# Kernel tuning notes

Measured on AMD Instinct MI355X. Metric: run time of the kernel, lower is better.

The kernel has to match this reference:

```python
import jax, jax.numpy as jnp
import numpy as np

N = 50000   # nodes
E = 800000  # edges
D = 128     # input feature dim
H = 128     # hidden dim
L = 3       # num GIN layers
G = 64      # graphs in batch


def setup_inputs() -> dict:
    key = jax.random.key(0)
    ks = jax.random.split(key, 20)
    inp = {
        "h": jax.random.normal(ks[0], (N, D), jnp.float32),
        "src": jax.random.randint(ks[1], (E,), 0, N),
        "dst": jax.random.randint(ks[2], (E,), 0, N),
        "graph_ids": jnp.sort(jax.random.randint(ks[3], (N,), 0, G)),
    }
    k = 4
    for i in range(L):
        in_dim = D if i == 0 else H
        inp[f"w1_{i}"] = jax.random.normal(ks[k], (in_dim, H), jnp.float32) / np.sqrt(in_dim).astype(np.float32); k += 1
        inp[f"b1_{i}"] = jnp.zeros((H,), jnp.float32)
        inp[f"w2_{i}"] = jax.random.normal(ks[k], (H, H), jnp.float32) / np.sqrt(H).astype(np.float32); k += 1
        inp[f"b2_{i}"] = jnp.zeros((H,), jnp.float32)
    inp["w_out"] = jax.random.normal(ks[k], (H * L, 1), jnp.float32) / np.sqrt(H * L).astype(np.float32)
    inp["b_out"] = jnp.zeros((1,), jnp.float32)
    return inp


def _gin_layer(h, src, dst, w1, b1, w2, b2):
    # sum aggregation over edges: agg[i] = sum_{(j->i) in E} h[j]
    agg = jax.ops.segment_sum(h[src], dst, num_segments=N)
    z = h + agg  # (1 + eps) * h + agg with eps = 0 (DGL GINConv default)
    return jax.nn.relu(z @ w1 + b1) @ w2 + b2  # 2-layer MLP


def reference(h, src, dst, graph_ids,
              w1_0, b1_0, w2_0, b2_0,
              w1_1, b1_1, w2_1, b2_1,
              w1_2, b1_2, w2_2, b2_2,
              w_out, b_out):
    layers = [(w1_0, b1_0, w2_0, b2_0),
              (w1_1, b1_1, w2_1, b2_1),
              (w1_2, b1_2, w2_2, b2_2)]
    readouts = []
    for w1, b1, w2, b2 in layers:
        h = _gin_layer(h, src, dst, w1, b1, w2, b2)
        # per-graph sum readout of node features: [G, H]
        readouts.append(jax.ops.segment_sum(h, graph_ids, num_segments=G))
    hg = jnp.concatenate(readouts, axis=1)  # [G, H*L]
    return hg @ w_out + b_out  # [G, 1]
```

## Files before the change

### kernel.cpp

```cpp
#include <hip/hip_runtime.h>

#define NN 50000
#define NE 800000
#define DIMH 128
#define NGRAPH 64
#define NTILES 3125
#define PAIRS 1024
#define MLP_BLOCKS 512
#define MLP_ITERS 4
#define NBIN 196
#define BCAP 8064

typedef __attribute__((ext_vector_type(8))) short bf16x8;
typedef __attribute__((ext_vector_type(4))) float f32x4;

__device__ __forceinline__ unsigned short f2b(float f) {
  unsigned int b = __float_as_uint(f);
  unsigned int r = (b + 0x7FFFu + ((b >> 16) & 1u)) >> 16;
  return (unsigned short)r;
}
__device__ __forceinline__ float b2f_lo(unsigned int u) { return __uint_as_float(u << 16); }
__device__ __forceinline__ float b2f_hi(unsigned int u) { return __uint_as_float(u & 0xffff0000u); }


__global__ void zero_int_kernel(int* __restrict__ p, int n) {
  int i = blockIdx.x * 256 + threadIdx.x;
  if (i < n) p[i] = 0;
}

__global__ __launch_bounds__(256) void bin_scatter_kernel(const int* __restrict__ src,
                                                          const int* __restrict__ dst,
                                                          int* __restrict__ gcnt,
                                                          int2* __restrict__ staging) {
  __shared__ int hist[NBIN];
  __shared__ int base[NBIN];
  int tid = threadIdx.x;
  for (int i = tid; i < NBIN; i += 256) hist[i] = 0;
  __syncthreads();
  int e0 = blockIdx.x * 2048;
  int2 ed[8];
  int bin[8], rank[8];
#pragma unroll
  for (int k = 0; k < 8; ++k) {
    int e = e0 + k * 256 + tid;
    bin[k] = 0; rank[k] = 0; ed[k] = make_int2(0, 0);
    if (e < NE) {
      ed[k].x = src[e]; ed[k].y = dst[e];
      bin[k] = ed[k].y >> 8;
      rank[k] = atomicAdd(&hist[bin[k]], 1);
    }
  }
  __syncthreads();
  for (int i = tid; i < NBIN; i += 256) base[i] = atomicAdd(&gcnt[i], hist[i]);
  __syncthreads();
#pragma unroll
  for (int k = 0; k < 8; ++k) {
    int e = e0 + k * 256 + tid;
    if (e < NE) staging[bin[k] * BCAP + base[bin[k]] + rank[k]] = ed[k];
  }
}

__global__ __launch_bounds__(256) void bin_fill_kernel(const int2* __restrict__ staging,
                                                       const int* __restrict__ gcnt,
                                                       int* __restrict__ bucket,
                                                       int* __restrict__ cnt) {
  __shared__ int h[256];
  int b = blockIdx.x;
  int tid = threadIdx.x;
  h[tid] = 0;
  __syncthreads();
  int n = gcnt[b];
  for (int i = tid; i < n; i += 256) {
    int2 e = staging[b * BCAP + i];
    int local = e.y & 255;
    int r = atomicAdd(&h[local], 1);
    if (r < 64) bucket[(b * 256 + local) * 64 + r] = e.x;
  }
  __syncthreads();
  int node = b * 256 + tid;
  if (node < NN) cnt[node] = h[tid];
}


__global__ void convw_kernel(const float* __restrict__ w, unsigned short* __restrict__ wt) {
  int i = blockIdx.x * 256 + threadIdx.x;
  int c = i >> 7, k = i & 127;
  wt[i] = f2b(w[k * DIMH + c]);
}

__global__ void convh_kernel(const float* __restrict__ h, unsigned int* __restrict__ o) {
  int i = blockIdx.x * 256 + threadIdx.x;
  float2 v = ((const float2*)h)[i];
  o[i] = (unsigned int)f2b(v.x) | ((unsigned int)f2b(v.y) << 16);
}


__global__ void agg_kernel(const uint2* __restrict__ hp, const int* __restrict__ cnt,
                           const int* __restrict__ bucket, uint2* __restrict__ z) {
  int gidx = blockIdx.x * 256 + threadIdx.x;
  int node = gidx >> 6;
  int lane = gidx & 63;
  int half = lane >> 5;
  int l5 = lane & 31;
  int c = cnt[node];
  if (c > 64) c = 64;
  int idx = bucket[node * 64 + lane];

  uint2 own = hp[node * 32 + l5];
  float a0 = b2f_lo(own.x), a1 = b2f_hi(own.x), a2 = b2f_lo(own.y), a3 = b2f_hi(own.y);
  if (half) { a0 = 0.f; a1 = 0.f; a2 = 0.f; a3 = 0.f; }

  int j = 0;
  for (; j + 8 <= c; j += 8) {
#pragma unroll
    for (int k = 0; k < 4; ++k) {
      int nb = __shfl(idx, j + 2 * k + half, 64);
      uint2 u = hp[nb * 32 + l5];
      a0 += b2f_lo(u.x); a1 += b2f_hi(u.x);
      a2 += b2f_lo(u.y); a3 += b2f_hi(u.y);
    }
  }
  for (; j < c; j += 2) {
    int slot = j + half;
    int s2 = slot < c ? slot : 0;
    int nb = __shfl(idx, s2, 64);
    uint2 u = hp[nb * 32 + l5];
    float m = slot < c ? 1.f : 0.f;
    a0 += m * b2f_lo(u.x); a1 += m * b2f_hi(u.x);
    a2 += m * b2f_lo(u.y); a3 += m * b2f_hi(u.y);
  }

  a0 += __shfl_xor(a0, 32, 64);
  a1 += __shfl_xor(a1, 32, 64);
  a2 += __shfl_xor(a2, 32, 64);
  a3 += __shfl_xor(a3, 32, 64);

  if (half == 0) {
    uint2 o;
    o.x = (unsigned int)f2b(a0) | ((unsigned int)f2b(a1) << 16);
    o.y = (unsigned int)f2b(a2) | ((unsigned int)f2b(a3) << 16);
    z[node * 32 + l5] = o;
  }
}

__global__ __launch_bounds__(256, 2) void mlp_kernel(const unsigned short* __restrict__ X,
                                                     const unsigned short* __restrict__ W1t,
                                                     const float* __restrict__ b1,
                                                     const unsigned short* __restrict__ W2t,
                                                     const float* __restrict__ b2,
                                                     unsigned short* __restrict__ Y,
                                                     const int* __restrict__ gids,
                                                     const float* __restrict__ wout,
                                                     float* __restrict__ gout) {
  __shared__ unsigned short y1[2][2][2048];
  __shared__ float s_gout[NGRAPH];
  int tid = threadIdx.x;
  if (tid < NGRAPH) s_gout[tid] = 0.f;

  int wv = tid >> 6;
  int lane = tid & 63;
  int pb = wv >> 1;
  int half = wv & 1;
  int l15 = lane & 15;
  int g = lane >> 4;
  int p = blockIdx.x * 2 + pb;

  bf16x8 a[4];
  {
    const unsigned short* xb = X + (p * 16 + l15) * DIMH + g * 8;
#pragma unroll
    for (int kt = 0; kt < 4; ++kt) a[kt] = *(const bf16x8*)(xb + kt * 32);
  }

  bf16x8 fb1[4][4], fb2[4][4];
  const unsigned short* w1b = W1t + (half * 64 + l15) * DIMH + g * 8;
  const unsigned short* w2b = W2t + (half * 64 + l15) * DIMH + g * 8;
#pragma unroll
  for (int n = 0; n < 4; ++n)
#pragma unroll
    for (int kt = 0; kt < 4; ++kt) {
      fb1[n][kt] = *(const bf16x8*)(w1b + n * 16 * DIMH + kt * 32);
      fb2[n][kt] = *(const bf16x8*)(w2b + n * 16 * DIMH + kt * 32);
    }
  float b1v[4], b2v[4], wov[4];
#pragma unroll
  for (int n = 0; n < 4; ++n) {
    int col = half * 64 + n * 16 + l15;
    b1v[n] = b1[col];
    b2v[n] = b2[col];
    wov[n] = wout[col];
  }
  __syncthreads();

#pragma unroll
  for (int i = 0; i < MLP_ITERS; ++i) {
    int rtc = p + i * PAIRS;
    bool active = rtc < NTILES;
    unsigned short* buf = y1[pb][i & 1];

    if (active) {
#pragma unroll
      for (int n = 0; n < 4; ++n) {
        f32x4 acc = (f32x4){0.f, 0.f, 0.f, 0.f};
#pragma unroll
        for (int kt = 0; kt < 4; ++kt)
          acc = __builtin_amdgcn_mfma_f32_16x16x32_bf16(a[kt], fb1[n][kt], acc, 0, 0, 0);
        int col2 = (half * 64 + n * 16 + l15) * 2;
#pragma unroll
        for (int r = 0; r < 4; ++r) {
          float f = fmaxf(acc[r] + b1v[n], 0.f);
          int row = 4 * g + r;
          buf[((row * 256 + col2) ^ (row << 4)) >> 1] = f2b(f);
        }
      }
    }

    int rtn = p + (i + 1) * PAIRS;
    if (i + 1 < MLP_ITERS && rtn < NTILES) {
      const unsigned short* xb = X + (rtn * 16 + l15) * DIMH + g * 8;
#pragma unroll
      for (int kt = 0; kt < 4; ++kt) a[kt] = *(const bf16x8*)(xb + kt * 32);
    }

    __syncthreads();

    if (active) {
      bf16x8 a2[4];
#pragma unroll
      for (int kt = 0; kt < 4; ++kt)
        a2[kt] = *(const bf16x8*)&buf[((l15 * 256 + kt * 64 + g * 16) ^ (l15 << 4)) >> 1];

      float pr[4] = {0.f, 0.f, 0.f, 0.f};
#pragma unroll
      for (int n = 0; n < 4; ++n) {
        f32x4 acc = (f32x4){0.f, 0.f, 0.f, 0.f};
#pragma unroll
        for (int kt = 0; kt < 4; ++kt)
          acc = __builtin_amdgcn_mfma_f32_16x16x32_bf16(a2[kt], fb2[n][kt], acc, 0, 0, 0);
        int col = half * 64 + n * 16 + l15;
#pragma unroll
        for (int r = 0; r < 4; ++r) {
          float f = acc[r] + b2v[n];
          if (Y) Y[(rtc * 16 + 4 * g + r) * DIMH + col] = f2b(f);
          pr[r] += f * wov[n];
        }
      }
#pragma unroll
      for (int r = 0; r < 4; ++r) {
#pragma unroll
        for (int off = 1; off < 16; off <<= 1) pr[r] += __shfl_xor(pr[r], off, 64);
      }
      if (l15 == 0) {
#pragma unroll
        for (int r = 0; r < 4; ++r)
          atomicAdd(&s_gout[gids[rtc * 16 + 4 * g + r]], pr[r]);
      }
    }
  }

  __syncthreads();
  if (tid < NGRAPH) {
    float v = s_gout[tid];
    if (v != 0.f) atomicAdd(&gout[tid], v);
  }
}

__global__ void init_out_kernel(float* __restrict__ out, const float* __restrict__ b_out) {
  int i = threadIdx.x;
  if (i < NGRAPH) out[i] = b_out[0];
}


extern "C" void kernel_launch(void* const* d_in, const int* in_sizes, int n_in,
                              void* d_out, int out_size, void* d_ws, size_t ws_size,
                              hipStream_t stream) {
  const float* h = (const float*)d_in[0];
  const int* src = (const int*)d_in[1];
  const int* dst = (const int*)d_in[2];
  const int* gids = (const int*)d_in[3];
  const float* w_out = (const float*)d_in[16];
  const float* b_out = (const float*)d_in[17];
  float* out = (float*)d_out;

  char* base = (char*)d_ws;
  unsigned int* bufH = (unsigned int*)(base);
  int2* staging = (int2*)(base + 12800000);
  unsigned int* bufC = (unsigned int*)(base + 25600000);
  int* bucket = (int*)(base + 38400000);
  int* cnt = (int*)(base + 51200000);
  int* gcnt = (int*)(base + 51400000);
  unsigned short* wt = (unsigned short*)(base + 51401024);

  zero_int_kernel<<<1, 256, 0, stream>>>(gcnt, NBIN);
  bin_scatter_kernel<<<(NE + 2047) / 2048, 256, 0, stream>>>(src, dst, gcnt, staging);
  bin_fill_kernel<<<NBIN, 256, 0, stream>>>(staging, gcnt, bucket, cnt);

  for (int l = 0; l < 3; ++l) {
    convw_kernel<<<64, 256, 0, stream>>>((const float*)d_in[4 + l * 4], wt + (2 * l) * 16384);
    convw_kernel<<<64, 256, 0, stream>>>((const float*)d_in[6 + l * 4], wt + (2 * l + 1) * 16384);
  }
  convh_kernel<<<(NN * 64) / 256, 256, 0, stream>>>(h, bufH);

  init_out_kernel<<<1, 64, 0, stream>>>(out, b_out);

  int agg_blocks = (NN * 64) / 256;

  for (int l = 0; l < 3; ++l) {
    const float* b1 = (const float*)d_in[5 + l * 4];
    const float* b2 = (const float*)d_in[7 + l * 4];
    const unsigned short* w1t = wt + (2 * l) * 16384;
    const unsigned short* w2t = wt + (2 * l + 1) * 16384;

    agg_kernel<<<agg_blocks, 256, 0, stream>>>((const uint2*)bufH, cnt, bucket, (uint2*)bufC);
    mlp_kernel<<<MLP_BLOCKS, 256, 0, stream>>>((const unsigned short*)bufC, w1t, b1, w2t, b2,
                                               (l == 2) ? nullptr : (unsigned short*)bufH,
                                               gids, w_out + l * DIMH, out);
  }
}
```

Measured before the change: 214.0 us.

## Fuse neighbor aggregation into MLP kernel and merge prep kernels

The edge-sum aggregation now runs inside the MLP kernel. Each block gathers neighbor rows for its 16-node tile into shared memory, so the aggregated tensor no longer makes a round trip through global memory. H is ping-ponged between two buffers across layers. The weight conversion, output init and counter zeroing are merged into one prep kernel to cut launches. In exchange, the gather is done with 8 threads per node and fewer waves per block, which may lower memory-level parallelism, and the previous prefetch of the next tile is dropped.

```diff
diff --git a/kernel.cpp b/kernel.cpp
--- a/kernel.cpp
+++ b/kernel.cpp
@@ -6,7 +6,6 @@
 #define NGRAPH 64
 #define NTILES 3125
 #define PAIRS 1024
-#define MLP_BLOCKS 512
 #define MLP_ITERS 4
 #define NBIN 196
 #define BCAP 8064
@@ -21,12 +20,20 @@
 }
 __device__ __forceinline__ float b2f_lo(unsigned int u) { return __uint_as_float(u << 16); }
 __device__ __forceinline__ float b2f_hi(unsigned int u) { return __uint_as_float(u & 0xffff0000u); }
-
-
-__global__ void zero_int_kernel(int* __restrict__ p, int n) {
-  int i = blockIdx.x * 256 + threadIdx.x;
-  if (i < n) p[i] = 0;
-}
+__device__ __forceinline__ unsigned int pk2(float lo, float hi) {
+  return (unsigned int)f2b(lo) | ((unsigned int)f2b(hi) << 16);
+}
+__device__ __forceinline__ void addrow(float* ac, uint4 u0, uint4 u1) {
+  ac[0] += b2f_lo(u0.x); ac[1] += b2f_hi(u0.x);
+  ac[2] += b2f_lo(u0.y); ac[3] += b2f_hi(u0.y);
+  ac[4] += b2f_lo(u0.z); ac[5] += b2f_hi(u0.z);
+  ac[6] += b2f_lo(u0.w); ac[7] += b2f_hi(u0.w);
+  ac[8] += b2f_lo(u1.x); ac[9] += b2f_hi(u1.x);
+  ac[10] += b2f_lo(u1.y); ac[11] += b2f_hi(u1.y);
+  ac[12] += b2f_lo(u1.z); ac[13] += b2f_hi(u1.z);
+  ac[14] += b2f_lo(u1.w); ac[15] += b2f_hi(u1.w);
+}
+
 
 __global__ __launch_bounds__(256) void bin_scatter_kernel(const int* __restrict__ src,
                                                           const int* __restrict__ dst,
@@ -82,95 +89,47 @@
 }
 
 
-__global__ void convw_kernel(const float* __restrict__ w, unsigned short* __restrict__ wt) {
+struct WPtrs { const float* w[6]; const float* b_out; };
+
+__global__ __launch_bounds__(256) void prep_kernel(WPtrs ptrs, unsigned short* __restrict__ wt,
+                                                   float* __restrict__ out,
+                                                   int* __restrict__ gcnt) {
   int i = blockIdx.x * 256 + threadIdx.x;
-  int c = i >> 7, k = i & 127;
-  wt[i] = f2b(w[k * DIMH + c]);
+  int m = i >> 14;
+  int idx = i & 16383;
+  int c = idx >> 7, k = idx & 127;
+  wt[m * 16384 + idx] = f2b(ptrs.w[m][k * DIMH + c]);
+  if (i < NGRAPH) out[i] = ptrs.b_out[0];
+  if (i < NBIN) gcnt[i] = 0;
 }
 
 __global__ void convh_kernel(const float* __restrict__ h, unsigned int* __restrict__ o) {
   int i = blockIdx.x * 256 + threadIdx.x;
   float2 v = ((const float2*)h)[i];
-  o[i] = (unsigned int)f2b(v.x) | ((unsigned int)f2b(v.y) << 16);
-}
-
-
-__global__ void agg_kernel(const uint2* __restrict__ hp, const int* __restrict__ cnt,
-                           const int* __restrict__ bucket, uint2* __restrict__ z) {
-  int gidx = blockIdx.x * 256 + threadIdx.x;
-  int node = gidx >> 6;
-  int lane = gidx & 63;
-  int half = lane >> 5;
-  int l5 = lane & 31;
-  int c = cnt[node];
-  if (c > 64) c = 64;
-  int idx = bucket[node * 64 + lane];
-
-  uint2 own = hp[node * 32 + l5];
-  float a0 = b2f_lo(own.x), a1 = b2f_hi(own.x), a2 = b2f_lo(own.y), a3 = b2f_hi(own.y);
-  if (half) { a0 = 0.f; a1 = 0.f; a2 = 0.f; a3 = 0.f; }
-
-  int j = 0;
-  for (; j + 8 <= c; j += 8) {
-#pragma unroll
-    for (int k = 0; k < 4; ++k) {
-      int nb = __shfl(idx, j + 2 * k + half, 64);
-      uint2 u = hp[nb * 32 + l5];
-      a0 += b2f_lo(u.x); a1 += b2f_hi(u.x);
-      a2 += b2f_lo(u.y); a3 += b2f_hi(u.y);
-    }
-  }
-  for (; j < c; j += 2) {
-    int slot = j + half;
-    int s2 = slot < c ? slot : 0;
-    int nb = __shfl(idx, s2, 64);
-    uint2 u = hp[nb * 32 + l5];
-    float m = slot < c ? 1.f : 0.f;
-    a0 += m * b2f_lo(u.x); a1 += m * b2f_hi(u.x);
-    a2 += m * b2f_lo(u.y); a3 += m * b2f_hi(u.y);
-  }
-
-  a0 += __shfl_xor(a0, 32, 64);
-  a1 += __shfl_xor(a1, 32, 64);
-  a2 += __shfl_xor(a2, 32, 64);
-  a3 += __shfl_xor(a3, 32, 64);
-
-  if (half == 0) {
-    uint2 o;
-    o.x = (unsigned int)f2b(a0) | ((unsigned int)f2b(a1) << 16);
-    o.y = (unsigned int)f2b(a2) | ((unsigned int)f2b(a3) << 16);
-    z[node * 32 + l5] = o;
-  }
-}
-
-__global__ __launch_bounds__(256, 2) void mlp_kernel(const unsigned short* __restrict__ X,
-                                                     const unsigned short* __restrict__ W1t,
-                                                     const float* __restrict__ b1,
-                                                     const unsigned short* __restrict__ W2t,
-                                                     const float* __restrict__ b2,
-                                                     unsigned short* __restrict__ Y,
-                                                     const int* __restrict__ gids,
-                                                     const float* __restrict__ wout,
-                                                     float* __restrict__ gout) {
-  __shared__ unsigned short y1[2][2][2048];
+  o[i] = pk2(v.x, v.y);
+}
+
+__global__ __launch_bounds__(128, 2) void mlp_fused_kernel(
+    const unsigned short* __restrict__ H, const int* __restrict__ cnt,
+    const int* __restrict__ bucket,
+    const unsigned short* __restrict__ W1t, const float* __restrict__ b1,
+    const unsigned short* __restrict__ W2t, const float* __restrict__ b2,
+    unsigned short* __restrict__ Y,
+    const int* __restrict__ gids, const float* __restrict__ wout,
+    float* __restrict__ gout) {
+  __shared__ unsigned short zt[2][2048];
+  __shared__ unsigned short y1[2][2048];
   __shared__ float s_gout[NGRAPH];
   int tid = threadIdx.x;
   if (tid < NGRAPH) s_gout[tid] = 0.f;
 
-  int wv = tid >> 6;
   int lane = tid & 63;
-  int pb = wv >> 1;
-  int half = wv & 1;
+  int half = tid >> 6;
   int l15 = lane & 15;
   int g = lane >> 4;
-  int p = blockIdx.x * 2 + pb;
-
-  bf16x8 a[4];
-  {
-    const unsigned short* xb = X + (p * 16 + l15) * DIMH + g * 8;
-#pragma unroll
-    for (int kt = 0; kt < 4; ++kt) a[kt] = *(const bf16x8*)(xb + kt * 32);
-  }
+  int r8 = tid >> 3;
+  int s8 = tid & 7;
+  int p = blockIdx.x;
 
   bf16x8 fb1[4][4], fb2[4][4];
   const unsigned short* w1b = W1t + (half * 64 + l15) * DIMH + g * 8;
@@ -196,9 +155,63 @@
   for (int i = 0; i < MLP_ITERS; ++i) {
     int rtc = p + i * PAIRS;
     bool active = rtc < NTILES;
-    unsigned short* buf = y1[pb][i & 1];
+    unsigned short* zb = zt[i & 1];
+    unsigned short* yb = y1[i & 1];
 
     if (active) {
+      int node = rtc * 16 + r8;
+      int c = cnt[node];
+      if (c > 64) c = 64;
+      const uint4* hb = (const uint4*)H;
+      float ac[16];
+      {
+        uint4 v0 = hb[node * 16 + s8 * 2];
+        uint4 v1 = hb[node * 16 + s8 * 2 + 1];
+        ac[0] = b2f_lo(v0.x); ac[1] = b2f_hi(v0.x);
+        ac[2] = b2f_lo(v0.y); ac[3] = b2f_hi(v0.y);
+        ac[4] = b2f_lo(v0.z); ac[5] = b2f_hi(v0.z);
+        ac[6] = b2f_lo(v0.w); ac[7] = b2f_hi(v0.w);
+        ac[8] = b2f_lo(v1.x); ac[9] = b2f_hi(v1.x);
+        ac[10] = b2f_lo(v1.y); ac[11] = b2f_hi(v1.y);
+        ac[12] = b2f_lo(v1.z); ac[13] = b2f_hi(v1.z);
+        ac[14] = b2f_lo(v1.w); ac[15] = b2f_hi(v1.w);
+      }
+      const int* bk = bucket + node * 64;
+      int j = 0;
+      for (; j + 4 <= c; j += 4) {
+        int n0 = bk[j], n1 = bk[j + 1], n2 = bk[j + 2], n3 = bk[j + 3];
+        uint4 a0 = hb[n0 * 16 + s8 * 2], a1 = hb[n0 * 16 + s8 * 2 + 1];
+        uint4 c0 = hb[n1 * 16 + s8 * 2], c1 = hb[n1 * 16 + s8 * 2 + 1];
+        uint4 d0 = hb[n2 * 16 + s8 * 2], d1 = hb[n2 * 16 + s8 * 2 + 1];
+        uint4 e0 = hb[n3 * 16 + s8 * 2], e1 = hb[n3 * 16 + s8 * 2 + 1];
+        addrow(ac, a0, a1);
+        addrow(ac, c0, c1);
+        addrow(ac, d0, d1);
+        addrow(ac, e0, e1);
+      }
+      for (; j < c; ++j) {
+        int nb = bk[j];
+        uint4 u0 = hb[nb * 16 + s8 * 2], u1 = hb[nb * 16 + s8 * 2 + 1];
+        addrow(ac, u0, u1);
+      }
+      uint4 o0, o1;
+      o0.x = pk2(ac[0], ac[1]);  o0.y = pk2(ac[2], ac[3]);
+      o0.z = pk2(ac[4], ac[5]);  o0.w = pk2(ac[6], ac[7]);
+      o1.x = pk2(ac[8], ac[9]);  o1.y = pk2(ac[10], ac[11]);
+      o1.z = pk2(ac[12], ac[13]); o1.w = pk2(ac[14], ac[15]);
+      int byte0 = (r8 * 256 + s8 * 32) ^ (r8 << 4);
+      *(uint4*)((char*)zb + byte0) = o0;
+      *(uint4*)((char*)zb + (byte0 ^ 16)) = o1;
+    }
+
+    __syncthreads();
+
+    if (active) {
+      bf16x8 a[4];
+#pragma unroll
+      for (int kt = 0; kt < 4; ++kt)
+        a[kt] = *(const bf16x8*)((const char*)zb +
+                                 ((l15 * 256 + kt * 64 + g * 16) ^ (l15 << 4)));
 #pragma unroll
       for (int n = 0; n < 4; ++n) {
         f32x4 acc = (f32x4){0.f, 0.f, 0.f, 0.f};
@@ -210,16 +223,9 @@
         for (int r = 0; r < 4; ++r) {
           float f = fmaxf(acc[r] + b1v[n], 0.f);
           int row = 4 * g + r;
-          buf[((row * 256 + col2) ^ (row << 4)) >> 1] = f2b(f);
+          yb[((row * 256 + col2) ^ (row << 4)) >> 1] = f2b(f);
         }
       }
-    }
-
-    int rtn = p + (i + 1) * PAIRS;
-    if (i + 1 < MLP_ITERS && rtn < NTILES) {
-      const unsigned short* xb = X + (rtn * 16 + l15) * DIMH + g * 8;
-#pragma unroll
-      for (int kt = 0; kt < 4; ++kt) a[kt] = *(const bf16x8*)(xb + kt * 32);
     }
 
     __syncthreads();
@@ -228,8 +234,8 @@
       bf16x8 a2[4];
 #pragma unroll
       for (int kt = 0; kt < 4; ++kt)
-        a2[kt] = *(const bf16x8*)&buf[((l15 * 256 + kt * 64 + g * 16) ^ (l15 << 4)) >> 1];
-
+        a2[kt] = *(const bf16x8*)((const char*)yb +
+                                  ((l15 * 256 + kt * 64 + g * 16) ^ (l15 << 4)));
       float pr[4] = {0.f, 0.f, 0.f, 0.f};
 #pragma unroll
       for (int n = 0; n < 4; ++n) {
@@ -263,11 +269,6 @@
     float v = s_gout[tid];
     if (v != 0.f) atomicAdd(&gout[tid], v);
   }
-}
-
-__global__ void init_out_kernel(float* __restrict__ out, const float* __restrict__ b_out) {
-  int i = threadIdx.x;
-  if (i < NGRAPH) out[i] = b_out[0];
 }
 
 
@@ -283,37 +284,35 @@
   float* out = (float*)d_out;
 
   char* base = (char*)d_ws;
-  unsigned int* bufH = (unsigned int*)(base);
-  int2* staging = (int2*)(base + 12800000);
-  unsigned int* bufC = (unsigned int*)(base + 25600000);
+  unsigned short* buf0 = (unsigned short*)(base);
+  unsigned short* buf1 = (unsigned short*)(base + 12800000);
+  int2* staging = (int2*)(base + 25600000);
   int* bucket = (int*)(base + 38400000);
   int* cnt = (int*)(base + 51200000);
-  int* gcnt = (int*)(base + 51400000);
+  int* gcnt = (int*)(base + 51400064);
   unsigned short* wt = (unsigned short*)(base + 51401024);
 
-  zero_int_kernel<<<1, 256, 0, stream>>>(gcnt, NBIN);
+  WPtrs ptrs;
+  for (int l = 0; l < 3; ++l) {
+    ptrs.w[2 * l] = (const float*)d_in[4 + l * 4];
+    ptrs.w[2 * l + 1] = (const float*)d_in[6 + l * 4];
+  }
+  ptrs.b_out = b_out;
+
+  prep_kernel<<<384, 256, 0, stream>>>(ptrs, wt, out, gcnt);
   bin_scatter_kernel<<<(NE + 2047) / 2048, 256, 0, stream>>>(src, dst, gcnt, staging);
   bin_fill_kernel<<<NBIN, 256, 0, stream>>>(staging, gcnt, bucket, cnt);
-
-  for (int l = 0; l < 3; ++l) {
-    convw_kernel<<<64, 256, 0, stream>>>((const float*)d_in[4 + l * 4], wt + (2 * l) * 16384);
-    convw_kernel<<<64, 256, 0, stream>>>((const float*)d_in[6 + l * 4], wt + (2 * l + 1) * 16384);
-  }
-  convh_kernel<<<(NN * 64) / 256, 256, 0, stream>>>(h, bufH);
-
-  init_out_kernel<<<1, 64, 0, stream>>>(out, b_out);
-
-  int agg_blocks = (NN * 64) / 256;
+  convh_kernel<<<(NN * 64) / 256, 256, 0, stream>>>(h, (unsigned int*)buf0);
 
   for (int l = 0; l < 3; ++l) {
     const float* b1 = (const float*)d_in[5 + l * 4];
     const float* b2 = (const float*)d_in[7 + l * 4];
-    const unsigned short* w1t = wt + (2 * l) * 16384;
-    const unsigned short* w2t = wt + (2 * l + 1) * 16384;
-
-    agg_kernel<<<agg_blocks, 256, 0, stream>>>((const uint2*)bufH, cnt, bucket, (uint2*)bufC);
-    mlp_kernel<<<MLP_BLOCKS, 256, 0, stream>>>((const unsigned short*)bufC, w1t, b1, w2t, b2,
-                                               (l == 2) ? nullptr : (unsigned short*)bufH,
-                                               gids, w_out + l * DIMH, out);
-  }
-}
+    const unsigned short* Hl = (l & 1) ? buf1 : buf0;
+    unsigned short* Yl = (l & 1) ? buf0 : buf1;
+    mlp_fused_kernel<<<PAIRS, 128, 0, stream>>>(
+        Hl, cnt, bucket,
+        wt + (2 * l) * 16384, b1, wt + (2 * l + 1) * 16384, b2,
+        (l == 2) ? nullptr : Yl,
+        gids, w_out + l * DIMH, out);
+  }
+}
```

Result: slower. 223.4 us (+4.4%).

## Slice node features into column blocks, build CSR adjacency, fuse prep kernels

Applied to the files above, without the earlier changes.

Stores node features in 8 column slices of 16 bf16 each, so every aggregation block gathers from a slice of about 1.6 MB that can stay cache-resident. Replaces the fixed 64-slot buckets with a compact CSR adjacency built from a per-bin prefix scan, which also drops the 64-neighbour cap. Merges the weight conversion, output init and counter zeroing into one prep kernel, and updates the MLP loads and stores to the sliced layout. The cost is 8x more aggregation blocks and per-slice re-reading of the adjacency indices.

```diff
diff --git a/kernel.cpp b/kernel.cpp
--- a/kernel.cpp
+++ b/kernel.cpp
@@ -10,6 +10,8 @@
 #define MLP_ITERS 4
 #define NBIN 196
 #define BCAP 8064
+#define SL_US 800000
+#define SL_U2 200000
 
 typedef __attribute__((ext_vector_type(8))) short bf16x8;
 typedef __attribute__((ext_vector_type(4))) float f32x4;
@@ -21,12 +23,10 @@
 }
 __device__ __forceinline__ float b2f_lo(unsigned int u) { return __uint_as_float(u << 16); }
 __device__ __forceinline__ float b2f_hi(unsigned int u) { return __uint_as_float(u & 0xffff0000u); }
-
-
-__global__ void zero_int_kernel(int* __restrict__ p, int n) {
-  int i = blockIdx.x * 256 + threadIdx.x;
-  if (i < n) p[i] = 0;
-}
+__device__ __forceinline__ unsigned int pk2(float lo, float hi) {
+  return (unsigned int)f2b(lo) | ((unsigned int)f2b(hi) << 16);
+}
+
 
 __global__ __launch_bounds__(256) void bin_scatter_kernel(const int* __restrict__ src,
                                                           const int* __restrict__ dst,
@@ -62,85 +62,110 @@
 
 __global__ __launch_bounds__(256) void bin_fill_kernel(const int2* __restrict__ staging,
                                                        const int* __restrict__ gcnt,
-                                                       int* __restrict__ bucket,
-                                                       int* __restrict__ cnt) {
-  __shared__ int h[256];
+                                                       int* __restrict__ adj,
+                                                       int* __restrict__ row_ptr,
+                                                       int* __restrict__ cnt,
+                                                       int* __restrict__ alloc) {
+  __shared__ int hdeg[256], loc[256], c2[256];
+  __shared__ int sbase;
   int b = blockIdx.x;
   int tid = threadIdx.x;
-  h[tid] = 0;
+  hdeg[tid] = 0; c2[tid] = 0;
   __syncthreads();
   int n = gcnt[b];
+  for (int i = tid; i < n; i += 256)
+    atomicAdd(&hdeg[staging[b * BCAP + i].y & 255], 1);
+  __syncthreads();
+  int v = hdeg[tid];
+  loc[tid] = v;
+  __syncthreads();
+  for (int off = 1; off < 256; off <<= 1) {
+    int t = (tid >= off) ? loc[tid - off] : 0;
+    __syncthreads();
+    loc[tid] += t;
+    __syncthreads();
+  }
+  if (tid == 255) sbase = atomicAdd(alloc, loc[255]);
+  __syncthreads();
+  int excl = loc[tid] - v;
+  int node = b * 256 + tid;
+  if (node < NN) { row_ptr[node] = sbase + excl; cnt[node] = v; }
+  loc[tid] = excl;
+  __syncthreads();
   for (int i = tid; i < n; i += 256) {
     int2 e = staging[b * BCAP + i];
     int local = e.y & 255;
-    int r = atomicAdd(&h[local], 1);
-    if (r < 64) bucket[(b * 256 + local) * 64 + r] = e.x;
-  }
-  __syncthreads();
-  int node = b * 256 + tid;
-  if (node < NN) cnt[node] = h[tid];
-}
-
-
-__global__ void convw_kernel(const float* __restrict__ w, unsigned short* __restrict__ wt) {
+    int r = atomicAdd(&c2[local], 1);
+    adj[sbase + loc[local] + r] = e.x;
+  }
+}
+
+
+struct WPtrs { const float* w[6]; const float* b_out; };
+
+__global__ __launch_bounds__(256) void prep_kernel(WPtrs ptrs, unsigned short* __restrict__ wt,
+                                                   float* __restrict__ out,
+                                                   int* __restrict__ gcnt,
+                                                   int* __restrict__ alloc) {
   int i = blockIdx.x * 256 + threadIdx.x;
-  int c = i >> 7, k = i & 127;
-  wt[i] = f2b(w[k * DIMH + c]);
-}
-
-__global__ void convh_kernel(const float* __restrict__ h, unsigned int* __restrict__ o) {
-  int i = blockIdx.x * 256 + threadIdx.x;
-  float2 v = ((const float2*)h)[i];
-  o[i] = (unsigned int)f2b(v.x) | ((unsigned int)f2b(v.y) << 16);
-}
-
-
-__global__ void agg_kernel(const uint2* __restrict__ hp, const int* __restrict__ cnt,
-                           const int* __restrict__ bucket, uint2* __restrict__ z) {
-  int gidx = blockIdx.x * 256 + threadIdx.x;
-  int node = gidx >> 6;
-  int lane = gidx & 63;
-  int half = lane >> 5;
-  int l5 = lane & 31;
+  int m = i >> 14;
+  int idx = i & 16383;
+  int c = idx >> 7, k = idx & 127;
+  wt[m * 16384 + idx] = f2b(ptrs.w[m][k * DIMH + c]);
+  if (i < NGRAPH) out[i] = ptrs.b_out[0];
+  if (i < NBIN) gcnt[i] = 0;
+  if (i == NBIN) *alloc = 0;
+}
+
+__global__ void convh_kernel(const float* __restrict__ h, uint2* __restrict__ Hs) {
+  int t = blockIdx.x * 256 + threadIdx.x;
+  int node = t >> 5;
+  int q = t & 31;
+  float4 v = *(const float4*)&h[node * DIMH + q * 4];
+  uint2 o;
+  o.x = pk2(v.x, v.y);
+  o.y = pk2(v.z, v.w);
+  Hs[(q >> 2) * SL_U2 + node * 4 + (q & 3)] = o;
+}
+
+__global__ __launch_bounds__(256) void agg_kernel(const uint2* __restrict__ Hs,
+                                                  const int* __restrict__ row_ptr,
+                                                  const int* __restrict__ cnt,
+                                                  const int* __restrict__ adj,
+                                                  uint2* __restrict__ Zs) {
+  int bid = blockIdx.x;
+  int slice = bid & 7;
+  int nb = bid >> 3;
+  int tid = threadIdx.x;
+  int node = nb * 64 + (tid >> 2);
+  int l4 = tid & 3;
+  if (node >= NN) return;
+  const uint2* hp = Hs + slice * SL_U2;
+  int start = row_ptr[node];
   int c = cnt[node];
-  if (c > 64) c = 64;
-  int idx = bucket[node * 64 + lane];
-
-  uint2 own = hp[node * 32 + l5];
+  uint2 own = hp[node * 4 + l4];
   float a0 = b2f_lo(own.x), a1 = b2f_hi(own.x), a2 = b2f_lo(own.y), a3 = b2f_hi(own.y);
-  if (half) { a0 = 0.f; a1 = 0.f; a2 = 0.f; a3 = 0.f; }
-
   int j = 0;
-  for (; j + 8 <= c; j += 8) {
-#pragma unroll
-    for (int k = 0; k < 4; ++k) {
-      int nb = __shfl(idx, j + 2 * k + half, 64);
-      uint2 u = hp[nb * 32 + l5];
-      a0 += b2f_lo(u.x); a1 += b2f_hi(u.x);
-      a2 += b2f_lo(u.y); a3 += b2f_hi(u.y);
-    }
-  }
-  for (; j < c; j += 2) {
-    int slot = j + half;
-    int s2 = slot < c ? slot : 0;
-    int nb = __shfl(idx, s2, 64);
-    uint2 u = hp[nb * 32 + l5];
-    float m = slot < c ? 1.f : 0.f;
-    a0 += m * b2f_lo(u.x); a1 += m * b2f_hi(u.x);
-    a2 += m * b2f_lo(u.y); a3 += m * b2f_hi(u.y);
-  }
-
-  a0 += __shfl_xor(a0, 32, 64);
-  a1 += __shfl_xor(a1, 32, 64);
-  a2 += __shfl_xor(a2, 32, 64);
-  a3 += __shfl_xor(a3, 32, 64);
-
-  if (half == 0) {
-    uint2 o;
-    o.x = (unsigned int)f2b(a0) | ((unsigned int)f2b(a1) << 16);
-    o.y = (unsigned int)f2b(a2) | ((unsigned int)f2b(a3) << 16);
-    z[node * 32 + l5] = o;
-  }
+  for (; j + 4 <= c; j += 4) {
+    int my = adj[start + j + l4];
+    int n0 = __shfl(my, 0, 4), n1 = __shfl(my, 1, 4);
+    int n2 = __shfl(my, 2, 4), n3 = __shfl(my, 3, 4);
+    uint2 u0 = hp[n0 * 4 + l4], u1 = hp[n1 * 4 + l4];
+    uint2 u2 = hp[n2 * 4 + l4], u3 = hp[n3 * 4 + l4];
+    a0 += b2f_lo(u0.x); a1 += b2f_hi(u0.x); a2 += b2f_lo(u0.y); a3 += b2f_hi(u0.y);
+    a0 += b2f_lo(u1.x); a1 += b2f_hi(u1.x); a2 += b2f_lo(u1.y); a3 += b2f_hi(u1.y);
+    a0 += b2f_lo(u2.x); a1 += b2f_hi(u2.x); a2 += b2f_lo(u2.y); a3 += b2f_hi(u2.y);
+    a0 += b2f_lo(u3.x); a1 += b2f_hi(u3.x); a2 += b2f_lo(u3.y); a3 += b2f_hi(u3.y);
+  }
+  for (; j < c; ++j) {
+    int nbr = adj[start + j];
+    uint2 u = hp[nbr * 4 + l4];
+    a0 += b2f_lo(u.x); a1 += b2f_hi(u.x); a2 += b2f_lo(u.y); a3 += b2f_hi(u.y);
+  }
+  uint2 o;
+  o.x = pk2(a0, a1);
+  o.y = pk2(a2, a3);
+  Zs[slice * SL_U2 + node * 4 + l4] = o;
 }
 
 __global__ __launch_bounds__(256, 2) void mlp_kernel(const unsigned short* __restrict__ X,
@@ -165,11 +190,14 @@
   int g = lane >> 4;
   int p = blockIdx.x * 2 + pb;
 
+  int asl_base = (g >> 1) * SL_US + (g & 1) * 8 + l15 * 16;
+
   bf16x8 a[4];
   {
-    const unsigned short* xb = X + (p * 16 + l15) * DIMH + g * 8;
-#pragma unroll
-    for (int kt = 0; kt < 4; ++kt) a[kt] = *(const bf16x8*)(xb + kt * 32);
+    int roff = p * 256;
+#pragma unroll
+    for (int kt = 0; kt < 4; ++kt)
+      a[kt] = *(const bf16x8*)(X + 2 * kt * SL_US + roff + asl_base);
   }
 
   bf16x8 fb1[4][4], fb2[4][4];
@@ -217,9 +245,10 @@
 
     int rtn = p + (i + 1) * PAIRS;
     if (i + 1 < MLP_ITERS && rtn < NTILES) {
-      const unsigned short* xb = X + (rtn * 16 + l15) * DIMH + g * 8;
-#pragma unroll
-      for (int kt = 0; kt < 4; ++kt) a[kt] = *(const bf16x8*)(xb + kt * 32);
+      int roff = rtn * 256;
+#pragma unroll
+      for (int kt = 0; kt < 4; ++kt)
+        a[kt] = *(const bf16x8*)(X + 2 * kt * SL_US + roff + asl_base);
     }
 
     __syncthreads();
@@ -237,11 +266,11 @@
 #pragma unroll
         for (int kt = 0; kt < 4; ++kt)
           acc = __builtin_amdgcn_mfma_f32_16x16x32_bf16(a2[kt], fb2[n][kt], acc, 0, 0, 0);
-        int col = half * 64 + n * 16 + l15;
+        int sl = 4 * half + n;
 #pragma unroll
         for (int r = 0; r < 4; ++r) {
           float f = acc[r] + b2v[n];
-          if (Y) Y[(rtc * 16 + 4 * g + r) * DIMH + col] = f2b(f);
+          if (Y) Y[sl * SL_US + (rtc * 16 + 4 * g + r) * 16 + l15] = f2b(f);
           pr[r] += f * wov[n];
         }
       }
@@ -263,11 +292,6 @@
     float v = s_gout[tid];
     if (v != 0.f) atomicAdd(&gout[tid], v);
   }
-}
-
-__global__ void init_out_kernel(float* __restrict__ out, const float* __restrict__ b_out) {
-  int i = threadIdx.x;
-  if (i < NGRAPH) out[i] = b_out[0];
 }
 
 
@@ -283,37 +307,42 @@
   float* out = (float*)d_out;
 
   char* base = (char*)d_ws;
-  unsigned int* bufH = (unsigned int*)(base);
-  int2* staging = (int2*)(base + 12800000);
-  unsigned int* bufC = (unsigned int*)(base + 25600000);
-  int* bucket = (int*)(base + 38400000);
-  int* cnt = (int*)(base + 51200000);
-  int* gcnt = (int*)(base + 51400000);
-  unsigned short* wt = (unsigned short*)(base + 51401024);
-
-  zero_int_kernel<<<1, 256, 0, stream>>>(gcnt, NBIN);
+  unsigned short* buf0 = (unsigned short*)(base);
+  unsigned short* buf1 = (unsigned short*)(base + 12800000);
+  int2* staging = (int2*)(base + 25600000);
+  int* adj = (int*)(base + 38400000);
+  int* row_ptr = (int*)(base + 41600000);
+  int* cnt = (int*)(base + 41800064);
+  int* gcnt = (int*)(base + 42000128);
+  int* alloc = (int*)(base + 42001024);
+  unsigned short* wt = (unsigned short*)(base + 42002048);
+
+  WPtrs ptrs;
+  for (int l = 0; l < 3; ++l) {
+    ptrs.w[2 * l] = (const float*)d_in[4 + l * 4];
+    ptrs.w[2 * l + 1] = (const float*)d_in[6 + l * 4];
+  }
+  ptrs.b_out = b_out;
+
+  prep_kernel<<<384, 256, 0, stream>>>(ptrs, wt, out, gcnt, alloc);
   bin_scatter_kernel<<<(NE + 2047) / 2048, 256, 0, stream>>>(src, dst, gcnt, staging);
-  bin_fill_kernel<<<NBIN, 256, 0, stream>>>(staging, gcnt, bucket, cnt);
-
-  for (int l = 0; l < 3; ++l) {
-    convw_kernel<<<64, 256, 0, stream>>>((const float*)d_in[4 + l * 4], wt + (2 * l) * 16384);
-    convw_kernel<<<64, 256, 0, stream>>>((const float*)d_in[6 + l * 4], wt + (2 * l + 1) * 16384);
-  }
-  convh_kernel<<<(NN * 64) / 256, 256, 0, stream>>>(h, bufH);
-
-  init_out_kernel<<<1, 64, 0, stream>>>(out, b_out);
-
-  int agg_blocks = (NN * 64) / 256;
+  bin_fill_kernel<<<NBIN, 256, 0, stream>>>(staging, gcnt, adj, row_ptr, cnt, alloc);
+  convh_kernel<<<(NN * 32) / 256 + 1, 256, 0, stream>>>(h, (uint2*)buf0);
+
+  int agg_blocks = 782 * 8;
 
   for (int l = 0; l < 3; ++l) {
     const float* b1 = (const float*)d_in[5 + l * 4];
     const float* b2 = (const float*)d_in[7 + l * 4];
-    const unsigned short* w1t = wt + (2 * l) * 16384;
-    const unsigned short* w2t = wt + (2 * l + 1) * 16384;
-
-    agg_kernel<<<agg_blocks, 256, 0, stream>>>((const uint2*)bufH, cnt, bucket, (uint2*)bufC);
-    mlp_kernel<<<MLP_BLOCKS, 256, 0, stream>>>((const unsigned short*)bufC, w1t, b1, w2t, b2,
-                                               (l == 2) ? nullptr : (unsigned short*)bufH,
+    const unsigned short* Hl = (l & 1) ? buf1 : buf0;
+    unsigned short* Yl = (l & 1) ? buf0 : buf1;
+    unsigned short* Zl = (unsigned short*)staging;
+    Zl = (unsigned short*)(base + 42300000);
+    agg_kernel<<<agg_blocks, 256, 0, stream>>>((const uint2*)Hl, row_ptr, cnt, adj,
+                                               (uint2*)Zl);
+    mlp_kernel<<<MLP_BLOCKS, 256, 0, stream>>>(Zl, wt + (2 * l) * 16384, b1,
+                                               wt + (2 * l + 1) * 16384, b2,
+                                               (l == 2) ? nullptr : Yl,
                                                gids, w_out + l * DIMH, out);
   }
 }
```

After: 225.1 us. +5.2%, slower.
